# Kernel optimization log

Measured on AMD Instinct MI355X. Metric: run time of the kernel, lower is better.

The kernel has to match this reference:

```python
import jax, jax.numpy as jnp
import numpy as np

WS = (5, 3, 1)          # per-level window sizes (CrossLayerPosEmbedding3D default)
STRIDES = (4, 2, 1)
PADS = (2, 1, 0)
HWS = (80, 40, 20)      # per-level map sizes -> 20x20 = 400 windows per level
B, C, NH = 8, 256, 4
HD = C // NH            # head_dim = 64
NTOK = (25, 9, 1)       # tokens per level, total 35
W0 = WS[0]
TABLE = (2 * W0 - 1) ** 2  # 81


def _rel_pos_index():
    # replicates CrossLayerPosEmbedding3D (spatial=True): float cross-scale coords
    coords = []
    for i, w in enumerate(WS):
        c = (np.arange(w) - w // 2).astype(np.float64)
        if i < len(WS) - 1:
            c = c * (W0 / w)
        gh, gw = np.meshgrid(c, c, indexing='ij')
        coords.append(np.stack([gh.reshape(-1), gw.reshape(-1)]))
    cf = np.concatenate(coords, axis=-1)                       # (2, 35)
    rel = (cf[:, :, None] - cf[:, None, :]).transpose(1, 2, 0).copy()
    rel[..., 0] += W0 - 1
    rel[..., 1] += W0 - 1
    rel[..., 0] *= 2 * W0 - 1
    return rel.sum(-1).astype(np.float32)                      # (35, 35) float index

REL_IDX = _rel_pos_index()
LEVEL_OF_TOKEN = np.repeat(np.arange(3), NTOK)                 # (35,)


def unfold(x, k, s, p):
    # torch.nn.functional.unfold -> (B, n_windows, k*k, C) (overlaped_window_partition)
    Bx, Cx, H, W = x.shape
    xp = jnp.pad(x, ((0, 0), (0, 0), (p, p), (p, p)))
    oh = (H + 2 * p - k) // s + 1
    ow = (W + 2 * p - k) // s + 1
    hi = (np.arange(oh) * s)[:, None] + np.arange(k)           # (oh, k)
    wi = (np.arange(ow) * s)[:, None] + np.arange(k)           # (ow, k)
    pt = xp[:, :, hi[:, None, :, None], wi[None, :, None, :]]  # (B, C, oh, ow, k, k)
    return pt.transpose(0, 2, 3, 4, 5, 1).reshape(Bx, oh * ow, k * k, Cx)


def fold(win, H, W, k, s, p):
    # torch.nn.functional.fold (sums overlaps) (overlaped_window_reverse)
    Bx, Wm, _, Cx = win.shape
    oh = (H + 2 * p - k) // s + 1
    ow = (W + 2 * p - k) // s + 1
    Hp, Wp = H + 2 * p, W + 2 * p
    hi = (np.arange(oh) * s)[:, None] + np.arange(k)
    wi = (np.arange(ow) * s)[:, None] + np.arange(k)
    lin = (hi[:, None, :, None] * Wp + wi[None, :, None, :]).reshape(-1)
    vals = win.transpose(0, 3, 1, 2).reshape(Bx, Cx, -1)       # matches (Wm, k*k) flatten order
    canvas = jnp.zeros((Bx, Cx, Hp * Wp), win.dtype).at[:, :, lin].add(vals)
    return canvas.reshape(Bx, Cx, Hp, Wp)[:, :, p:p + H, p:p + W]


def _l2n(x):
    # F.normalize(dim=-1), eps=1e-12
    return x / jnp.maximum(jnp.linalg.norm(x, axis=-1, keepdims=True), 1e-12)


def _forward(x0, x1, x2, w_qkv0, w_qkv1, w_qkv2, w_proj, b_proj, rpb_table, abs_bias):
    xs = (x0, x1, x2)
    wq = (w_qkv0, w_qkv1, w_qkv2)
    qs, ks, vs = [], [], []
    for l in range(3):  # small fixed layer loop (structurally distinct weights)
        t = unfold(xs[l], WS[l], STRIDES[l], PADS[l])          # (B, 400, ws^2, C)
        qkv = jnp.einsum('bwtc,cf->bwtf', t, wq[l])
        Bx, Wm, T, _ = qkv.shape
        qkv = qkv.reshape(Bx, Wm, T, 3, NH, HD).transpose(3, 0, 4, 1, 2, 5)  # (3,B,H,Wm,t,hd)
        qs.append(qkv[0]); ks.append(qkv[1]); vs.append(qkv[2])
    q = jnp.concatenate(qs, axis=-2)                           # (B, H, 400, 35, hd)
    k = jnp.concatenate(ks, axis=-2)
    v = jnp.concatenate(vs, axis=-2)

    # interpolated cross-layer relative position bias (floor/ceil lerp on the table)
    idx = jnp.asarray(REL_IDX.reshape(-1))
    fl = jnp.clip(jnp.floor(idx).astype(jnp.int32), 0, TABLE - 1)
    ce = jnp.clip(jnp.ceil(idx).astype(jnp.int32), 0, TABLE - 1)
    wce = (idx - fl.astype(jnp.float32))[:, None]
    pos = (1.0 - wce) * rpb_table[fl] + wce * rpb_table[ce]    # (1225, NH)
    pos = pos.reshape(sum(NTOK), sum(NTOK), NH).transpose(2, 0, 1)  # (NH, 35, 35)
    # per-level absolute bias added on query-row blocks (torch cat over dim=-2)
    pos = pos + abs_bias[LEVEL_OF_TOKEN].T[:, :, None]

    attn = jnp.einsum('bhwqd,bhwkd->bhwqk', _l2n(q), _l2n(k)) + pos[None, :, None]
    attn = jax.nn.softmax(attn, axis=-1)
    out = jnp.einsum('bhwqk,bhwkd->bhwqd', attn, v)            # (B, H, 400, 35, hd)
    Bx = out.shape[0]
    out = out.transpose(0, 2, 3, 1, 4).reshape(Bx, -1, sum(NTOK), NH * HD)  # (B,400,35,C)
    out = jnp.einsum('bwtc,cf->bwtf', out, w_proj) + b_proj
    outs = jnp.split(out, np.cumsum(NTOK)[:-1].tolist(), axis=2)
    return tuple(fold(o, HWS[l], HWS[l], WS[l], STRIDES[l], PADS[l])
                 for l, o in enumerate(outs))


def setup_inputs() -> dict:
    key = jax.random.key(0)
    ks = jax.random.split(key, 8)
    return {
        'x0': jax.random.normal(ks[0], (B, C, 80, 80), jnp.float32),
        'x1': jax.random.normal(ks[1], (B, C, 40, 40), jnp.float32),
        'x2': jax.random.normal(ks[2], (B, C, 20, 20), jnp.float32),
        'w_qkv0': jax.random.normal(ks[3], (C, 3 * C), jnp.float32) * 0.02,
        'w_qkv1': jax.random.normal(ks[4], (C, 3 * C), jnp.float32) * 0.02,
        'w_qkv2': jax.random.normal(ks[5], (C, 3 * C), jnp.float32) * 0.02,
        'w_proj': jax.random.normal(ks[6], (C, C), jnp.float32) * 0.02,
        'b_proj': jnp.zeros((C,), jnp.float32),
        'rpb_table': jax.random.normal(ks[7], (TABLE, NH), jnp.float32) * 0.02,
        'abs_bias': jnp.zeros((3, NH), jnp.float32),
    }


def reference(x0, x1, x2, w_qkv0, w_qkv1, w_qkv2, w_proj, b_proj, rpb_table, abs_bias):
    return _forward(x0, x1, x2, w_qkv0, w_qkv1, w_qkv2, w_proj, b_proj, rpb_table, abs_bias)
```

## Files before the change

### kernel.cpp

```cpp
#include <hip/hip_runtime.h>
#include <math.h>

namespace {

typedef _Float16 half8v __attribute__((ext_vector_type(8)));
typedef _Float16 half4v __attribute__((ext_vector_type(4)));
typedef float    floatx4 __attribute__((ext_vector_type(4)));

constexpr int B   = 8;
constexpr int C   = 256;
constexpr int NH  = 4;
constexpr int HD  = 64;
constexpr int NWIN = 400;
constexpr int NT  = 35;
constexpr int QKVN = 768;
constexpr int RPB = NWIN * NT;

constexpr size_t QKV_B  = (size_t)8400 * QKVN * 2;
constexpr size_t OATT_B = (size_t)RPB * C * 2;
constexpr size_t YT_B   = (size_t)RPB * C * 4;
constexpr size_t PB_B   = QKV_B + OATT_B + YT_B;
constexpr size_t WT_B   = (size_t)3 * QKVN * C * 2;
constexpr size_t POS_B  = 19712;

__device__ inline void token_coord(int j, double& cy, double& cx) {
  if (j < 25)      { int ty = j / 5,  tx = j % 5;  cy = (double)(ty - 2); cx = (double)(tx - 2); }
  else if (j < 34) { int t = j - 25; int ty = t / 3, tx = t % 3;
                     cy = (double)(ty - 1) * (5.0 / 3.0); cx = (double)(tx - 1) * (5.0 / 3.0); }
  else             { cy = 0.0; cx = 0.0; }
}

__global__ void pos_kernel(const float* __restrict__ rpb, const float* __restrict__ ab,
                           float* __restrict__ pos) {
  int p = blockIdx.x * blockDim.x + threadIdx.x;
  if (p >= NH * NT * NT) return;
  int j = p % NT, i = (p / NT) % NT, h = p / (NT * NT);
  double cyi, cxi, cyj, cxj;
  token_coord(i, cyi, cxi);
  token_coord(j, cyj, cxj);
  float fidx = (float)(((cyi - cyj) + 4.0) * 9.0 + ((cxi - cxj) + 4.0));
  int fl = min(max((int)floorf(fidx), 0), 80);
  int ce = min(max((int)ceilf(fidx), 0), 80);
  float w = fidx - (float)fl;
  float pv = (1.0f - w) * rpb[fl * NH + h] + w * rpb[ce * NH + h];
  int li = (i < 25) ? 0 : ((i < 34) ? 1 : 2);
  pos[p] = pv + ab[li * NH + h];
}

__global__ __launch_bounds__(256) void wt_kernel(const float* __restrict__ w0,
                                                 const float* __restrict__ w1,
                                                 const float* __restrict__ w2,
                                                 _Float16* __restrict__ wt) {
  const int bx = blockIdx.x;
  const float* src = bx < 12 ? w0 : (bx < 24 ? w1 : w2);
  _Float16* dst = wt + (size_t)(bx / 12) * QKVN * C;
  const int m0 = (bx % 12) * 64;
  __shared__ _Float16 t[64][264];
  const int tid = threadIdx.x;
  const int p4 = (tid & 15) * 4;
#pragma unroll
  for (int it = 0; it < 16; ++it) {
    int c = it * 16 + (tid >> 4);
    floatx4 v = *(const floatx4*)(src + (size_t)c * QKVN + m0 + p4);
#pragma unroll
    for (int i = 0; i < 4; ++i) t[p4 + i][c] = (_Float16)v[i];
  }
  __syncthreads();
#pragma unroll
  for (int e0 = 0; e0 < 8; ++e0) {
    int e = e0 * 256 + tid;
    int p = e >> 5, c8 = e & 31;
    *(half8v*)(dst + (size_t)(m0 + p) * C + c8 * 8) = *(const half8v*)&t[p][c8 * 8];
  }
}

__global__ __launch_bounds__(256) void qkv_gemm(const float* __restrict__ X0,
                                                const float* __restrict__ X1,
                                                const float* __restrict__ X2,
                                                const _Float16* __restrict__ Wt,
                                                _Float16* __restrict__ Y0,
                                                _Float16* __restrict__ Y1,
                                                _Float16* __restrict__ Y2,
                                                int mb0, int mb01, int g) {
  __shared__ _Float16 As[128][264];
  __shared__ _Float16 Bs[128][40];

  int mblk = blockIdx.x;
  const float* X; const _Float16* WtL; _Float16* Y; int HW;
  if (mblk < mb0)       { X = X0; WtL = Wt;                 Y = Y0; HW = 6400; }
  else if (mblk < mb01) { X = X1; WtL = Wt + QKVN * C;      Y = Y1; HW = 1600; mblk -= mb0; }
  else                  { X = X2; WtL = Wt + 2 * QKVN * C;  Y = Y2; HW =  400; mblk -= mb01; }
  const int Mg = g * HW;

  const int tid  = threadIdx.x;
  const int m0   = mblk * 128;
  const int w    = tid >> 6;
  const int lane = tid & 63;
  const int quad = lane >> 4;
  const int mn   = lane & 15;

  {
    const int r  = tid & 127;
    const int ob = tid >> 7;
    int gm = min(m0 + r, Mg - 1);
    int bb = gm / HW, pix = gm - bb * HW;
    const float* xb = X + (size_t)bb * C * HW + pix;
#pragma unroll
    for (int i = 0; i < 16; ++i) {
      int oct = ob + 2 * i;
      const float* xp = xb + (size_t)oct * 8 * HW;
      half8v hv;
#pragma unroll
      for (int j = 0; j < 8; ++j) hv[j] = (_Float16)xp[(size_t)j * HW];
      *(half8v*)&As[r][oct * 8] = hv;
    }
  }

  int rr[2], k8[2];
#pragma unroll
  for (int u = 0; u < 2; ++u) { int e = u * 256 + tid; rr[u] = e >> 2; k8[u] = e & 3; }

  half8v bpre[2];
  auto PLOAD = [&](int nt, int k0) {
#pragma unroll
    for (int u = 0; u < 2; ++u)
      bpre[u] = *(const half8v*)(WtL + (size_t)(nt * 128 + rr[u]) * C + k8[u] * 8 + k0);
  };

  PLOAD(0, 0);
  __syncthreads();

  for (int nt = 0; nt < 6; ++nt) {
    floatx4 acc[2][8] = {};
    for (int k0 = 0; k0 < C; k0 += 32) {
#pragma unroll
      for (int u = 0; u < 2; ++u) *(half8v*)&Bs[rr[u]][k8[u] * 8] = bpre[u];
      __syncthreads();
      int nk = k0 + 32, nn = nt;
      if (nk == C) { nk = 0; nn = nt + 1; }
      if (nn < 6) PLOAD(nn, nk);
      half8v a0 = *(const half8v*)&As[w * 32 + mn][k0 + quad * 8];
      half8v a1 = *(const half8v*)&As[w * 32 + 16 + mn][k0 + quad * 8];
#pragma unroll
      for (int ni = 0; ni < 8; ++ni) {
        half8v bf = *(const half8v*)&Bs[ni * 16 + mn][quad * 8];
        acc[0][ni] = __builtin_amdgcn_mfma_f32_16x16x32_f16(a0, bf, acc[0][ni], 0, 0, 0);
        acc[1][ni] = __builtin_amdgcn_mfma_f32_16x16x32_f16(a1, bf, acc[1][ni], 0, 0, 0);
      }
      __syncthreads();
    }

    const int n0 = nt * 128;
    const bool do_norm = (n0 < 512);
#pragma unroll
    for (int mi = 0; mi < 2; ++mi) {
#pragma unroll
      for (int r = 0; r < 4; ++r) {
        float s0 = 0.f, s1 = 0.f;
#pragma unroll
        for (int ni = 0; ni < 4; ++ni) { float vv = acc[mi][ni][r]; s0 += vv * vv; }
#pragma unroll
        for (int ni = 4; ni < 8; ++ni) { float vv = acc[mi][ni][r]; s1 += vv * vv; }
        s0 += __shfl_xor(s0, 1); s1 += __shfl_xor(s1, 1);
        s0 += __shfl_xor(s0, 2); s1 += __shfl_xor(s1, 2);
        s0 += __shfl_xor(s0, 4); s1 += __shfl_xor(s1, 4);
        s0 += __shfl_xor(s0, 8); s1 += __shfl_xor(s1, 8);
        float sc0 = do_norm ? (1.f / fmaxf(sqrtf(s0), 1e-12f)) : 1.f;
        float sc1 = do_norm ? (1.f / fmaxf(sqrtf(s1), 1e-12f)) : 1.f;
        int row = m0 + w * 32 + mi * 16 + quad * 4 + r;
        if (row < Mg) {
#pragma unroll
          for (int ni = 0; ni < 8; ++ni)
            Y[(size_t)row * QKVN + n0 + ni * 16 + mn] =
                (_Float16)(acc[mi][ni][r] * (ni < 4 ? sc0 : sc1));
        }
      }
    }
  }
}

__device__ inline const _Float16* token_row_ptr(int j, int wy, int wx, int b,
                                                const _Float16* q0, const _Float16* q1,
                                                const _Float16* q2) {
  if (j >= NT) return nullptr;
  int k_, s_, p_, Hl, t; const _Float16* base;
  if (j < 25)      { k_ = 5; s_ = 4; p_ = 2; Hl = 80; t = j;      base = q0; }
  else if (j < 34) { k_ = 3; s_ = 2; p_ = 1; Hl = 40; t = j - 25; base = q1; }
  else             { k_ = 1; s_ = 1; p_ = 0; Hl = 20; t = 0;      base = q2; }
  int ty = t / k_, tx = t % k_;
  int y = wy * s_ + ty - p_;
  int x = wx * s_ + tx - p_;
  if ((unsigned)y >= (unsigned)Hl || (unsigned)x >= (unsigned)Hl) return nullptr;
  return base + ((size_t)b * Hl * Hl + (size_t)y * Hl + x) * QKVN;
}

__global__ __launch_bounds__(256, 4) void attn_kernel(const _Float16* __restrict__ qkv0,
                                                      const _Float16* __restrict__ qkv1,
                                                      const _Float16* __restrict__ qkv2,
                                                      const float* __restrict__ pos,
                                                      _Float16* __restrict__ O) {
  const int blk = blockIdx.x;
  const int w   = blk % NWIN;
  const int b   = blk / NWIN;
  const int wy = w / 20, wx = w % 20;
  const int tid  = threadIdx.x;
  const int h    = tid >> 6;
  const int lane = tid & 63;
  const int i16  = lane & 15;
  const int q4   = lane >> 4;

  __shared__ __align__(16) _Float16 vrows[48][260];

#pragma unroll
  for (int e0 = 0; e0 < 1536; e0 += 256) {
    int e = e0 + tid;
    int j = e >> 5, cc = e & 31;
    half8v val = (half8v)(_Float16)0.f;
    if (j < NT) {
      const _Float16* rp = token_row_ptr(j, wy, wx, b, qkv0, qkv1, qkv2);
      if (rp) val = *(const half8v*)(rp + 512 + cc * 8);
    }
    *(half8v*)&vrows[j][cc * 8] = val;
  }

  half8v qf[3][2], kf[3][2];
#pragma unroll
  for (int t = 0; t < 3; ++t) {
    const _Float16* rp = token_row_ptr(t * 16 + i16, wy, wx, b, qkv0, qkv1, qkv2);
#pragma unroll
    for (int kc = 0; kc < 2; ++kc) {
      if (rp) {
        qf[t][kc] = *(const half8v*)(rp + h * HD + kc * 32 + q4 * 8);
        kf[t][kc] = *(const half8v*)(rp + 256 + h * HD + kc * 32 + q4 * 8);
      } else {
        qf[t][kc] = (half8v)(_Float16)0.f;
        kf[t][kc] = (half8v)(_Float16)0.f;
      }
    }
  }

  floatx4 s[3][3] = {};
#pragma unroll
  for (int kc = 0; kc < 2; ++kc)
#pragma unroll
    for (int tj = 0; tj < 3; ++tj)
#pragma unroll
      for (int ti = 0; ti < 3; ++ti)
        s[tj][ti] = __builtin_amdgcn_mfma_f32_16x16x32_f16(kf[tj][kc], qf[ti][kc], s[tj][ti], 0, 0, 0);

#pragma unroll
  for (int tj = 0; tj < 3; ++tj)
#pragma unroll
    for (int ti = 0; ti < 3; ++ti)
#pragma unroll
      for (int r = 0; r < 4; ++r) {
        int j = tj * 16 + q4 * 4 + r;
        int i = ti * 16 + i16;
        if (j < NT) { if (i < NT) s[tj][ti][r] += pos[(h * NT + i) * NT + j]; }
        else s[tj][ti][r] = -INFINITY;
      }

  half4v pa[3][3];
#pragma unroll
  for (int ti = 0; ti < 3; ++ti) {
    float m = s[0][ti][0];
#pragma unroll
    for (int tj = 0; tj < 3; ++tj)
#pragma unroll
      for (int r = 0; r < 4; ++r) m = fmaxf(m, s[tj][ti][r]);
    m = fmaxf(m, __shfl_xor(m, 16));
    m = fmaxf(m, __shfl_xor(m, 32));
    float sum = 0.f;
#pragma unroll
    for (int tj = 0; tj < 3; ++tj)
#pragma unroll
      for (int r = 0; r < 4; ++r) { float e = expf(s[tj][ti][r] - m); s[tj][ti][r] = e; sum += e; }
    sum += __shfl_xor(sum, 16);
    sum += __shfl_xor(sum, 32);
    float inv = 1.f / sum;
#pragma unroll
    for (int tj = 0; tj < 3; ++tj)
#pragma unroll
      for (int r = 0; r < 4; ++r) pa[tj][ti][r] = (_Float16)(s[tj][ti][r] * inv);
  }

  __syncthreads();

  half4v vb[3][4];
#pragma unroll
  for (int tj = 0; tj < 3; ++tj)
#pragma unroll
    for (int n = 0; n < 4; ++n)
#pragma unroll
      for (int kk = 0; kk < 4; ++kk)
        vb[tj][n][kk] = vrows[tj * 16 + q4 * 4 + kk][h * HD + n * 16 + i16];

  const size_t obase = ((size_t)(b * NWIN + w) * NT) * C + h * HD;
#pragma unroll
  for (int ti = 0; ti < 3; ++ti) {
    floatx4 o[4] = {};
#pragma unroll
    for (int tj = 0; tj < 3; ++tj)
#pragma unroll
      for (int n = 0; n < 4; ++n)
        o[n] = __builtin_amdgcn_mfma_f32_16x16x16f16(pa[tj][ti], vb[tj][n], o[n], 0, 0, 0);
#pragma unroll
    for (int r = 0; r < 4; ++r) {
      int i = ti * 16 + q4 * 4 + r;
      if (i < NT) {
#pragma unroll
        for (int n = 0; n < 4; ++n)
          O[obase + (size_t)i * C + n * 16 + i16] = (_Float16)o[n][r];
      }
    }
  }
}

__global__ __launch_bounds__(256) void proj_gemm(const _Float16* __restrict__ A,
                                                 const float* __restrict__ W,
                                                 const float* __restrict__ bias,
                                                 float* __restrict__ Yt, int Mg) {
  __shared__ __align__(16) char smem[128 * 69 * 4];
  _Float16 (*As)[40] = (_Float16(*)[40])smem;
  _Float16 (*Bs)[40] = (_Float16(*)[40])(smem + 128 * 40 * 2);
  float    (*Cs)[69] = (float(*)[69])smem;

  const int tid  = threadIdx.x;
  const int m0   = blockIdx.x * 128;
  const int n0   = blockIdx.y * 64;
  const int w    = tid >> 6;
  const int lane = tid & 63;
  const int quad = lane >> 4;
  const int mn   = lane & 15;

  int aM[2], aK8[2], aRow[2];
#pragma unroll
  for (int u = 0; u < 2; ++u) {
    int e = u * 256 + tid;
    aM[u] = e >> 2; aK8[u] = e & 3;
    aRow[u] = min(m0 + aM[u], Mg - 1);
  }

  half8v apre[2]; float bpre[8];
  auto PLOAD = [&](int k0) {
#pragma unroll
    for (int u = 0; u < 2; ++u)
      apre[u] = *(const half8v*)&A[(size_t)aRow[u] * C + k0 + 8 * aK8[u]];
    const float* wp = W + (size_t)(k0 + w * 8) * C + n0 + lane;
#pragma unroll
    for (int j = 0; j < 8; ++j) bpre[j] = wp[(size_t)j * C];
  };

  PLOAD(0);
  floatx4 acc[2][4] = {};
  for (int k0 = 0; k0 < C; k0 += 32) {
#pragma unroll
    for (int u = 0; u < 2; ++u) *(half8v*)&As[aM[u]][8 * aK8[u]] = apre[u];
    {
      half8v hv;
#pragma unroll
      for (int j = 0; j < 8; ++j) hv[j] = (_Float16)bpre[j];
      *(half8v*)&Bs[lane][w * 8] = hv;
    }
    __syncthreads();
    if (k0 + 32 < C) PLOAD(k0 + 32);
    half8v a0 = *(const half8v*)&As[w * 32 + mn][quad * 8];
    half8v a1 = *(const half8v*)&As[w * 32 + 16 + mn][quad * 8];
#pragma unroll
    for (int ni = 0; ni < 4; ++ni) {
      half8v bf = *(const half8v*)&Bs[ni * 16 + mn][quad * 8];
      acc[0][ni] = __builtin_amdgcn_mfma_f32_16x16x32_f16(a0, bf, acc[0][ni], 0, 0, 0);
      acc[1][ni] = __builtin_amdgcn_mfma_f32_16x16x32_f16(a1, bf, acc[1][ni], 0, 0, 0);
    }
    __syncthreads();
  }

#pragma unroll
  for (int mi = 0; mi < 2; ++mi)
#pragma unroll
    for (int r = 0; r < 4; ++r)
#pragma unroll
      for (int ni = 0; ni < 4; ++ni)
        Cs[w * 32 + mi * 16 + quad * 4 + r][ni * 16 + mn] =
            acc[mi][ni][r] + bias[n0 + ni * 16 + mn];
  __syncthreads();
#pragma unroll
  for (int u = 0; u < 32; ++u) {
    int e = u * 256 + tid;
    int ml = e & 127, cl = e >> 7;
    int m = m0 + ml;
    if (m < Mg) {
      int bb = m / RPB;
      int r = m - bb * RPB;
      Yt[((size_t)bb * C + n0 + cl) * RPB + r] = Cs[ml][cl];
    }
  }
}

__global__ __launch_bounds__(256) void fold_kernel(const float* __restrict__ Yt,
                                                   float* __restrict__ out,
                                                   int k_, int s_, int p_, int H_,
                                                   int toff, int total) {
  int idx = blockIdx.x * 256 + threadIdx.x;
  if (idx >= total) return;
  int x = idx % H_;
  int y = (idx / H_) % H_;
  int c = (idx / (H_ * H_)) % C;
  int b = idx / (C * H_ * H_);
  int py = y + p_, px = x + p_;
  int ay = py - k_ + 1;
  int wy_lo = ay <= 0 ? 0 : (ay + s_ - 1) / s_;
  int wy_hi = min(19, py / s_);
  int ax = px - k_ + 1;
  int wx_lo = ax <= 0 ? 0 : (ax + s_ - 1) / s_;
  int wx_hi = min(19, px / s_);
  const float* base = Yt + ((size_t)b * C + c) * RPB;
  float acc = 0.f;
  for (int wy = wy_lo; wy <= wy_hi; ++wy) {
    int tyy = py - wy * s_;
    for (int wx = wx_lo; wx <= wx_hi; ++wx) {
      int txx = px - wx * s_;
      acc += base[(wy * 20 + wx) * NT + toff + tyy * k_ + txx];
    }
  }
  out[idx] = acc;
}

}

extern "C" void kernel_launch(void* const* d_in, const int* in_sizes, int n_in,
                              void* d_out, int out_size, void* d_ws, size_t ws_size,
                              hipStream_t stream) {
  const float* x0    = (const float*)d_in[0];
  const float* x1    = (const float*)d_in[1];
  const float* x2    = (const float*)d_in[2];
  const float* wq0   = (const float*)d_in[3];
  const float* wq1   = (const float*)d_in[4];
  const float* wq2   = (const float*)d_in[5];
  const float* wproj = (const float*)d_in[6];
  const float* bproj = (const float*)d_in[7];
  const float* rpb   = (const float*)d_in[8];
  const float* ab    = (const float*)d_in[9];
  float* out = (float*)d_out;

  int g = 8;
  while (g > 1 && POS_B + (size_t)g * PB_B + WT_B > ws_size) g >>= 1;

  char* ws = (char*)d_ws;
  float*    posb  = (float*)ws;
  _Float16* qkv0g = (_Float16*)(ws + POS_B);
  _Float16* qkv1g = qkv0g + (size_t)g * 6400 * QKVN;
  _Float16* qkv2g = qkv1g + (size_t)g * 1600 * QKVN;
  _Float16* oatt  = qkv2g + (size_t)g *  400 * QKVN;
  float*    yt    = (float*)(ws + POS_B + (size_t)g * (QKV_B + OATT_B));
  _Float16* wt    = (_Float16*)(ws + POS_B + (size_t)g * PB_B);

  pos_kernel<<<(NH * NT * NT + 255) / 256, 256, 0, stream>>>(rpb, ab, posb);
  wt_kernel<<<36, 256, 0, stream>>>(wq0, wq1, wq2, wt);

  const size_t off1 = (size_t)B * C * 6400;
  const size_t off2 = off1 + (size_t)B * C * 1600;

  const int mb0 = (g * 6400 + 127) / 128;
  const int mb1 = (g * 1600 + 127) / 128;
  const int mb2 = (g *  400 + 127) / 128;

  for (int b0 = 0; b0 < B; b0 += g) {
    const float* x0g = x0 + (size_t)b0 * C * 6400;
    const float* x1g = x1 + (size_t)b0 * C * 1600;
    const float* x2g = x2 + (size_t)b0 * C * 400;

    qkv_gemm<<<mb0 + mb1 + mb2, 256, 0, stream>>>(
        x0g, x1g, x2g, wt, qkv0g, qkv1g, qkv2g, mb0, mb0 + mb1, g);

    attn_kernel<<<g * NWIN, 256, 0, stream>>>(qkv0g, qkv1g, qkv2g, posb, oatt);

    proj_gemm<<<dim3((g * RPB + 127) / 128, C / 64), 256, 0, stream>>>(oatt, wproj, bproj, yt, g * RPB);

    const int tot0 = g * C * 6400;
    const int tot1 = g * C * 1600;
    const int tot2 = g * C * 400;
    fold_kernel<<<(tot0 + 255) / 256, 256, 0, stream>>>(yt, out + (size_t)b0 * C * 6400,        5, 4, 2, 80, 0,  tot0);
    fold_kernel<<<(tot1 + 255) / 256, 256, 0, stream>>>(yt, out + off1 + (size_t)b0 * C * 1600, 3, 2, 1, 40, 25, tot1);
    fold_kernel<<<(tot2 + 255) / 256, 256, 0, stream>>>(yt, out + off2 + (size_t)b0 * C * 400,  1, 1, 0, 20, 34, tot2);
  }
}
```

Measured before the change: 474.4 us.

## Shrink QKV GEMM M-tile, split N across blocks, double-buffer B tiles

The QKV projection GEMM now uses 64-row M tiles instead of 128 and splits the six 128-column N tiles into two halves handled by separate blocks along a new grid dimension. This gives more blocks and less LDS per block, aiming for higher occupancy and better load balance. The B staging buffer is double-buffered so the next tile can be written while the current one is consumed, removing one barrier per k-step. In exchange, each input X tile is read and converted to fp16 twice, once per N half, and each wave issues fewer MFMAs per B fragment load.

```diff
diff --git a/kernel.cpp b/kernel.cpp
--- a/kernel.cpp
+++ b/kernel.cpp
@@ -82,10 +82,11 @@
                                                 _Float16* __restrict__ Y1,
                                                 _Float16* __restrict__ Y2,
                                                 int mb0, int mb01, int g) {
-  __shared__ _Float16 As[128][264];
-  __shared__ _Float16 Bs[128][40];
-
-  int mblk = blockIdx.x;
+  __shared__ _Float16 As[64][264];
+  __shared__ _Float16 Bs[2][128][40];
+
+  int mblk = blockIdx.y;
+  const int ny = blockIdx.x;
   const float* X; const _Float16* WtL; _Float16* Y; int HW;
   if (mblk < mb0)       { X = X0; WtL = Wt;                 Y = Y0; HW = 6400; }
   else if (mblk < mb01) { X = X1; WtL = Wt + QKVN * C;      Y = Y1; HW = 1600; mblk -= mb0; }
@@ -93,21 +94,21 @@
   const int Mg = g * HW;
 
   const int tid  = threadIdx.x;
-  const int m0   = mblk * 128;
+  const int m0   = mblk * 64;
   const int w    = tid >> 6;
   const int lane = tid & 63;
   const int quad = lane >> 4;
   const int mn   = lane & 15;
 
   {
-    const int r  = tid & 127;
-    const int ob = tid >> 7;
+    const int r  = tid & 63;
+    const int ob = tid >> 6;
     int gm = min(m0 + r, Mg - 1);
     int bb = gm / HW, pix = gm - bb * HW;
     const float* xb = X + (size_t)bb * C * HW + pix;
 #pragma unroll
-    for (int i = 0; i < 16; ++i) {
-      int oct = ob + 2 * i;
+    for (int i = 0; i < 8; ++i) {
+      int oct = ob + 4 * i;
       const float* xp = xb + (size_t)oct * 8 * HW;
       half8v hv;
 #pragma unroll
@@ -120,60 +121,61 @@
 #pragma unroll
   for (int u = 0; u < 2; ++u) { int e = u * 256 + tid; rr[u] = e >> 2; k8[u] = e & 3; }
 
+  const int nt0 = ny * 3;
   half8v bpre[2];
-  auto PLOAD = [&](int nt, int k0) {
+  auto PLOAD = [&](int st) {
+    int nt = nt0 + (st >> 3);
+    int k0 = (st & 7) * 32;
 #pragma unroll
     for (int u = 0; u < 2; ++u)
       bpre[u] = *(const half8v*)(WtL + (size_t)(nt * 128 + rr[u]) * C + k8[u] * 8 + k0);
   };
 
-  PLOAD(0, 0);
+  PLOAD(0);
+#pragma unroll
+  for (int u = 0; u < 2; ++u) *(half8v*)&Bs[0][rr[u]][k8[u] * 8] = bpre[u];
+  PLOAD(1);
   __syncthreads();
 
-  for (int nt = 0; nt < 6; ++nt) {
-    floatx4 acc[2][8] = {};
+  int cur = 0;
+  for (int nt = nt0; nt < nt0 + 3; ++nt) {
+    floatx4 acc[8] = {};
     for (int k0 = 0; k0 < C; k0 += 32) {
 #pragma unroll
-      for (int u = 0; u < 2; ++u) *(half8v*)&Bs[rr[u]][k8[u] * 8] = bpre[u];
-      __syncthreads();
-      int nk = k0 + 32, nn = nt;
-      if (nk == C) { nk = 0; nn = nt + 1; }
-      if (nn < 6) PLOAD(nn, nk);
-      half8v a0 = *(const half8v*)&As[w * 32 + mn][k0 + quad * 8];
-      half8v a1 = *(const half8v*)&As[w * 32 + 16 + mn][k0 + quad * 8];
+      for (int u = 0; u < 2; ++u) *(half8v*)&Bs[cur ^ 1][rr[u]][k8[u] * 8] = bpre[u];
+      int st2 = (nt - nt0) * 8 + (k0 >> 5) + 2;
+      if (st2 < 24) PLOAD(st2);
+      half8v a0 = *(const half8v*)&As[w * 16 + mn][k0 + quad * 8];
 #pragma unroll
       for (int ni = 0; ni < 8; ++ni) {
-        half8v bf = *(const half8v*)&Bs[ni * 16 + mn][quad * 8];
-        acc[0][ni] = __builtin_amdgcn_mfma_f32_16x16x32_f16(a0, bf, acc[0][ni], 0, 0, 0);
-        acc[1][ni] = __builtin_amdgcn_mfma_f32_16x16x32_f16(a1, bf, acc[1][ni], 0, 0, 0);
+        half8v bf = *(const half8v*)&Bs[cur][ni * 16 + mn][quad * 8];
+        acc[ni] = __builtin_amdgcn_mfma_f32_16x16x32_f16(a0, bf, acc[ni], 0, 0, 0);
       }
+      cur ^= 1;
       __syncthreads();
     }
 
     const int n0 = nt * 128;
     const bool do_norm = (n0 < 512);
 #pragma unroll
-    for (int mi = 0; mi < 2; ++mi) {
-#pragma unroll
-      for (int r = 0; r < 4; ++r) {
-        float s0 = 0.f, s1 = 0.f;
-#pragma unroll
-        for (int ni = 0; ni < 4; ++ni) { float vv = acc[mi][ni][r]; s0 += vv * vv; }
-#pragma unroll
-        for (int ni = 4; ni < 8; ++ni) { float vv = acc[mi][ni][r]; s1 += vv * vv; }
-        s0 += __shfl_xor(s0, 1); s1 += __shfl_xor(s1, 1);
-        s0 += __shfl_xor(s0, 2); s1 += __shfl_xor(s1, 2);
-        s0 += __shfl_xor(s0, 4); s1 += __shfl_xor(s1, 4);
-        s0 += __shfl_xor(s0, 8); s1 += __shfl_xor(s1, 8);
-        float sc0 = do_norm ? (1.f / fmaxf(sqrtf(s0), 1e-12f)) : 1.f;
-        float sc1 = do_norm ? (1.f / fmaxf(sqrtf(s1), 1e-12f)) : 1.f;
-        int row = m0 + w * 32 + mi * 16 + quad * 4 + r;
-        if (row < Mg) {
-#pragma unroll
-          for (int ni = 0; ni < 8; ++ni)
-            Y[(size_t)row * QKVN + n0 + ni * 16 + mn] =
-                (_Float16)(acc[mi][ni][r] * (ni < 4 ? sc0 : sc1));
-        }
+    for (int r = 0; r < 4; ++r) {
+      float s0 = 0.f, s1 = 0.f;
+#pragma unroll
+      for (int ni = 0; ni < 4; ++ni) { float vv = acc[ni][r]; s0 += vv * vv; }
+#pragma unroll
+      for (int ni = 4; ni < 8; ++ni) { float vv = acc[ni][r]; s1 += vv * vv; }
+      s0 += __shfl_xor(s0, 1); s1 += __shfl_xor(s1, 1);
+      s0 += __shfl_xor(s0, 2); s1 += __shfl_xor(s1, 2);
+      s0 += __shfl_xor(s0, 4); s1 += __shfl_xor(s1, 4);
+      s0 += __shfl_xor(s0, 8); s1 += __shfl_xor(s1, 8);
+      float sc0 = do_norm ? (1.f / fmaxf(sqrtf(s0), 1e-12f)) : 1.f;
+      float sc1 = do_norm ? (1.f / fmaxf(sqrtf(s1), 1e-12f)) : 1.f;
+      int row = m0 + w * 16 + quad * 4 + r;
+      if (row < Mg) {
+#pragma unroll
+        for (int ni = 0; ni < 8; ++ni)
+          Y[(size_t)row * QKVN + n0 + ni * 16 + mn] =
+              (_Float16)(acc[ni][r] * (ni < 4 ? sc0 : sc1));
       }
     }
   }
@@ -461,16 +463,16 @@
   const size_t off1 = (size_t)B * C * 6400;
   const size_t off2 = off1 + (size_t)B * C * 1600;
 
-  const int mb0 = (g * 6400 + 127) / 128;
-  const int mb1 = (g * 1600 + 127) / 128;
-  const int mb2 = (g *  400 + 127) / 128;
+  const int mb0 = (g * 6400 + 63) / 64;
+  const int mb1 = (g * 1600 + 63) / 64;
+  const int mb2 = (g *  400 + 63) / 64;
 
   for (int b0 = 0; b0 < B; b0 += g) {
     const float* x0g = x0 + (size_t)b0 * C * 6400;
     const float* x1g = x1 + (size_t)b0 * C * 1600;
     const float* x2g = x2 + (size_t)b0 * C * 400;
 
-    qkv_gemm<<<mb0 + mb1 + mb2, 256, 0, stream>>>(
+    qkv_gemm<<<dim3(2, mb0 + mb1 + mb2), 256, 0, stream>>>(
         x0g, x1g, x2g, wt, qkv0g, qkv1g, qkv2g, mb0, mb0 + mb1, g);
 
     attn_kernel<<<g * NWIN, 256, 0, stream>>>(qkv0g, qkv1g, qkv2g, posb, oatt);
```

New measurement: 468.6 us. Within noise of the previous version (-1.2%).
